# Optimization experiments

Hardware: AMD Instinct MI355X
Metric: run time of the kernel (lower is better)

Reference implementation:

```python
import jax, jax.numpy as jnp
import numpy as np

# RVQECell configuration (matches init_kwargs)
I_SZ, W_SZ, STAGES, ORDER, DEGREE = 6, 12, 3, 2, 2
BIAS = float(np.pi / 2)
ANC = ORDER - 1                      # ancillas_for_order(order) = order - 1
N = I_SZ + W_SZ + ANC                # 19 qubits
B = 32
INOUT = list(range(I_SZ))            # lanes 0..5
WORK = list(range(I_SZ, I_SZ + W_SZ))  # lanes 6..17
C_CTRL = I_SZ + W_SZ - 1             # controls per neuron = 17


def setup_inputs() -> dict:
    key = jax.random.key(0)
    ks = jax.random.split(key, 9)
    s = 0.1  # small init keeps neuron angles in a well-conditioned range
    psi = jax.random.normal(ks[0], (B, 2 ** N), jnp.float32)
    psi = psi / jnp.linalg.norm(psi, axis=1, keepdims=True)  # normalized kets
    return {
        "batch": psi,
        "w_in1": jax.random.normal(ks[1], (W_SZ, C_CTRL), jnp.float32) * s,
        "w_in2": jax.random.normal(ks[2], (W_SZ, C_CTRL, C_CTRL), jnp.float32) * s,
        "w_u": jax.random.normal(ks[3], (STAGES, W_SZ), jnp.float32) * s,
        "w_k1": jax.random.normal(ks[4], (STAGES, W_SZ, C_CTRL), jnp.float32) * s,
        "w_k2": jax.random.normal(ks[5], (STAGES, W_SZ, C_CTRL, C_CTRL), jnp.float32) * s,
        "w_out1": jax.random.normal(ks[6], (I_SZ, C_CTRL), jnp.float32) * s,
        "w_out2": jax.random.normal(ks[7], (I_SZ, C_CTRL, C_CTRL), jnp.float32) * s,
        "inputs": jax.random.randint(ks[8], (B, I_SZ), 0, 2, dtype=jnp.int32),
    }


def _rot_y(state, lane, alpha):
    # real rotation [[cos a, -sin a], [sin a, cos a]] on qubit `lane`.
    ax = lane + 1  # +1 for batch axis; state shape [B] + [2]*N
    c, s = jnp.cos(alpha), jnp.sin(alpha)
    p0 = jax.lax.index_in_dim(state, 0, ax, keepdims=True)
    p1 = jax.lax.index_in_dim(state, 1, ax, keepdims=True)
    return jnp.concatenate([c * p0 - s * p1, s * p0 + c * p1], axis=ax)


def _neuron(state, outlane, th1, th2):
    # Fast (deterministic RUS) quantum neuron of given ORDER/DEGREE:
    # per control-basis-branch rotation of `outlane` by alpha(x),
    # phi(x) = bias + sum_i th1_i x_i + sum_{i<j} th2_ij x_i x_j (degree 2),
    # alpha = q^(order-1)(phi), q(t) = arctan(tan(t)^2), stable via arctan2.
    controls = [l for l in range(I_SZ + W_SZ) if l != outlane]
    Cn = len(controls)
    x = jnp.arange(2 ** Cn)
    shifts = jnp.arange(Cn - 1, -1, -1)
    bits = ((x[:, None] >> shifts[None, :]) & 1).astype(state.dtype)  # [2^Cn, Cn]
    phi = BIAS + bits @ th1
    if DEGREE >= 2:
        phi = phi + jnp.einsum('xi,ij,xj->x', bits, jnp.triu(th2, 1), bits)
    alpha = phi
    for _ in range(ORDER - 1):
        alpha = jnp.arctan2(jnp.sin(alpha) ** 2, jnp.cos(alpha) ** 2)
    shape = [1] + [2 if l in controls else 1 for l in range(N)]
    return _rot_y(state, outlane, alpha.reshape(shape))


def _bitflip(state_flat, inputs):
    # Vectorized batched BitFlipLayer: X on inout lane i where inputs[b,i]==1,
    # i.e. permute amplitudes by XOR of the flip mask (lane 0 most significant).
    shifts = (N - 1) - jnp.arange(I_SZ)
    f = jnp.sum(inputs.astype(jnp.int32) << shifts[None, :], axis=1)  # [B]
    idx = jnp.arange(2 ** N, dtype=jnp.int32)[None, :] ^ f[:, None]
    return jnp.take_along_axis(state_flat, idx, axis=1)


def reference(batch, w_in1, w_in2, w_u, w_k1, w_k2, w_out1, w_out2, inputs):
    psi = _bitflip(batch, inputs).reshape((B,) + (2,) * N)
    # input layer: one neuron per workspace lane
    for j, out in enumerate(WORK):
        psi = _neuron(psi, out, w_in1[j], w_in2[j])
    # kernel layer: stages x (UnitaryLayer(workspace) + neurons)
    for st in range(STAGES):
        for j, lane in enumerate(WORK):
            psi = _rot_y(psi, lane, w_u[st, j])
        for j, out in enumerate(WORK):
            psi = _neuron(psi, out, w_k1[st, j], w_k2[st, j])
    psi = _bitflip(psi.reshape(B, -1), inputs).reshape((B,) + (2,) * N)
    # output layer: one neuron per inout lane
    for j, out in enumerate(INOUT):
        psi = _neuron(psi, out, w_out1[j], w_out2[j])
    # measurement probabilities over inout lanes: marginal of |amp|^2
    probs = jnp.sum(psi ** 2, axis=tuple(range(1 + I_SZ, 1 + N))).reshape(B, -1)
    return probs, psi.reshape(B, -1)
```

## Files before the change

### kernel.cpp

```cpp
#include <hip/hip_runtime.h>
#include <math.h>


#define BIAS_F 1.57079632679489662f

typedef float v4f __attribute__((ext_vector_type(4)));

__device__ __forceinline__ float4 ntload4(const float* p) {
    v4f v = __builtin_nontemporal_load((const v4f*)p);
    return make_float4(v.x, v.y, v.z, v.w);
}
__device__ __forceinline__ void ntstore4(float* p, float4 f) {
    v4f v = {f.x, f.y, f.z, f.w};
    __builtin_nontemporal_store(v, (v4f*)p);
}

__device__ __forceinline__ int SW(int i) { return i ^ ((i >> 3) & 0x1C); }
__device__ __forceinline__ float4 ldsld4(const float* st, int i) {
    return *(const float4*)&st[SW(i)];
}
__device__ __forceinline__ void ldsst4(float* st, int i, float4 v) {
    *(float4*)&st[SW(i)] = v;
}

__device__ __forceinline__ float2 dec(float v) {
    float t = sqrtf(fmaf(-v, v, 1.0f));
    float c = v >= 0.f ? v : t;
    float s = v >= 0.f ? t : -v;
    return make_float2(c, s);
}
#define LD2(p) (*(const float2*)(p))
#define LD4(p) (*(const float4*)(p))

__device__ __forceinline__ void rot4(float4& A, float4& B, float4 e) {
    float ax = A.x, ay = A.y, az = A.z, aw = A.w;
    A.x = e.x * ax - e.y * B.x;  B.x = e.y * ax + e.x * B.x;
    A.y = e.x * ay - e.y * B.y;  B.y = e.y * ay + e.x * B.y;
    A.z = e.z * az - e.w * B.z;  B.z = e.w * az + e.z * B.z;
    A.w = e.z * aw - e.w * B.w;  B.w = e.w * aw + e.z * B.w;
}
__device__ __forceinline__ void rotq(float4& P, float c, float s) {
    float px = P.x, py = P.y;
    P.x = c * px - s * P.z;  P.z = s * px + c * P.z;
    P.y = c * py - s * P.w;  P.w = s * py + c * P.w;
}

#define TABU_FLOATS (48u * 131072u * 2u)

__global__ __launch_bounds__(256) void tables_kernel(
    const float* __restrict__ w_in1, const float* __restrict__ w_in2,
    const float* __restrict__ w_k1,  const float* __restrict__ w_k2,
    const float* __restrict__ w_out1, const float* __restrict__ w_out2,
    float* __restrict__ tab)
{
    const int n = blockIdx.y;
    const int hi = blockIdx.x;
    const int tid = threadIdx.x;
    const float* th1;
    const float* th2;
    if (n < 12)      { th1 = w_in1 + n * 17;         th2 = w_in2 + n * 289; }
    else if (n < 48) { th1 = w_k1 + (n - 12) * 17;   th2 = w_k2 + (n - 12) * 289; }
    else             { th1 = w_out1 + (n - 48) * 17; th2 = w_out2 + (n - 48) * 289; }

    float bu[9], bt[8];
#pragma unroll
    for (int i = 0; i < 9; ++i) bu[i] = (float)((hi >> (8 - i)) & 1);
#pragma unroll
    for (int j = 0; j < 8; ++j) bt[j] = (float)((tid >> (7 - j)) & 1);

    float phi = BIAS_F;
#pragma unroll
    for (int i = 0; i < 9; ++i) {
        float acc = th1[i];
#pragma unroll
        for (int j = i + 1; j < 9; ++j) acc += bu[j] * th2[i * 17 + j];
#pragma unroll
        for (int j = 0; j < 8; ++j)     acc += bt[j] * th2[i * 17 + 9 + j];
        phi += bu[i] * acc;
    }
#pragma unroll
    for (int a = 0; a < 8; ++a) {
        float acc = th1[9 + a];
#pragma unroll
        for (int b2 = a + 1; b2 < 8; ++b2) acc += bt[b2] * th2[(9 + a) * 17 + 9 + b2];
        phi += bt[a] * acc;
    }
    float sp, cp;
    sincosf(phi, &sp, &cp);
    float c2 = cp * cp, s2 = sp * sp;
    float d = c2 * c2 + s2 * s2;
    float r = rsqrtf(d);
    r = r * (1.5f - 0.5f * d * r * r);
    float ca = c2 * r, sa = s2 * r;
    const int idx = (hi << 8) | tid;
    if (n < 48) {
        float2* p = (float2*)tab + ((size_t)n * 131072 + idx);
        *p = make_float2(ca, sa);
    } else {
        tab[TABU_FLOATS + (size_t)(n - 48) * 131072 + idx] = (ca <= sa) ? ca : -sa;
    }
}

template <int PA, bool NEUR>
__device__ __forceinline__ void pass_hi2(float* l0, float* l1, int t8,
    const float* tA, const float* tB, const float* tC,
    float cA, float sA, float cB, float sB, float cC, float sC)
{
    const int lowb = PA - 4;
    const int low = t8 & ((1 << lowb) - 1);
    const int high = t8 >> lowb;
    const int i0 = (high << (PA + 1)) | (low << 2);
    const int x0 = (high << (PA - 1)) | (low << 1);
    const int oa = 1 << PA, ob = oa >> 1, oc = oa >> 2;
    const int dhi = oa >> 2, dlo = oa >> 3;
    float4 ea00, ea01, ea10, ea11, eb00, eb01, eb10, eb11, ec00, ec01, ec10, ec11;
    if (NEUR) {
        ea00 = LD4(&tA[2 * x0]);            ea01 = LD4(&tA[2 * (x0 + dlo)]);
        ea10 = LD4(&tA[2 * (x0 + dhi)]);    ea11 = LD4(&tA[2 * (x0 + dhi + dlo)]);
        eb00 = LD4(&tB[2 * x0]);            eb01 = LD4(&tB[2 * (x0 + dlo)]);
        eb10 = LD4(&tB[2 * (x0 + dhi)]);    eb11 = LD4(&tB[2 * (x0 + dhi + dlo)]);
        ec00 = LD4(&tC[2 * x0]);            ec01 = LD4(&tC[2 * (x0 + dlo)]);
        ec10 = LD4(&tC[2 * (x0 + dhi)]);    ec11 = LD4(&tC[2 * (x0 + dhi + dlo)]);
    } else {
        ea00 = ea01 = ea10 = ea11 = make_float4(cA, sA, cA, sA);
        eb00 = eb01 = eb10 = eb11 = make_float4(cB, sB, cB, sB);
        ec00 = ec01 = ec10 = ec11 = make_float4(cC, sC, cC, sC);
    }
#pragma unroll
    for (int s = 0; s < 2; ++s) {
        float* sl = (s == 0) ? l0 : l1;
        float4 Q000 = ldsld4(sl, i0),            Q001 = ldsld4(sl, i0 + oc);
        float4 Q010 = ldsld4(sl, i0 + ob),       Q011 = ldsld4(sl, i0 + ob + oc);
        float4 Q100 = ldsld4(sl, i0 + oa),       Q101 = ldsld4(sl, i0 + oa + oc);
        float4 Q110 = ldsld4(sl, i0 + oa + ob),  Q111 = ldsld4(sl, i0 + oa + ob + oc);
        rot4(Q000, Q100, ea00); rot4(Q001, Q101, ea01);
        rot4(Q010, Q110, ea10); rot4(Q011, Q111, ea11);
        rot4(Q000, Q010, eb00); rot4(Q001, Q011, eb01);
        rot4(Q100, Q110, eb10); rot4(Q101, Q111, eb11);
        rot4(Q000, Q001, ec00); rot4(Q010, Q011, ec01);
        rot4(Q100, Q101, ec10); rot4(Q110, Q111, ec11);
        ldsst4(sl, i0, Q000);            ldsst4(sl, i0 + oc, Q001);
        ldsst4(sl, i0 + ob, Q010);       ldsst4(sl, i0 + ob + oc, Q011);
        ldsst4(sl, i0 + oa, Q100);       ldsst4(sl, i0 + oa + oc, Q101);
        ldsst4(sl, i0 + oa + ob, Q110);  ldsst4(sl, i0 + oa + ob + oc, Q111);
    }
}

template <bool NEUR>
__device__ __forceinline__ void pass_lo2(float* l0, float* l1, int t8,
    const float* tA, const float* tB, const float* tC,
    float cA, float sA, float cB, float sB, float cC, float sC)
{
    const int i0 = t8 << 5, x0 = t8 << 3;
    float4 ea0, ea1, ea2, ea3, eb0, eb1, eb2, eb3, ec0, ec1, ec2, ec3;
    if (NEUR) {
        ea0 = LD4(&tA[2 * x0]);      ea1 = LD4(&tA[2 * x0 + 4]);
        ea2 = LD4(&tA[2 * x0 + 8]);  ea3 = LD4(&tA[2 * x0 + 12]);
        eb0 = LD4(&tB[2 * x0]);      eb1 = LD4(&tB[2 * x0 + 4]);
        eb2 = LD4(&tB[2 * x0 + 8]);  eb3 = LD4(&tB[2 * x0 + 12]);
        ec0 = LD4(&tC[2 * x0]);      ec1 = LD4(&tC[2 * x0 + 4]);
        ec2 = LD4(&tC[2 * x0 + 8]);  ec3 = LD4(&tC[2 * x0 + 12]);
    } else {
        ea0 = ea1 = ea2 = ea3 = make_float4(cA, sA, cA, sA);
        eb0 = eb1 = eb2 = eb3 = make_float4(cB, sB, cB, sB);
        ec0 = ec1 = ec2 = ec3 = make_float4(cC, sC, cC, sC);
    }
#pragma unroll
    for (int s = 0; s < 2; ++s) {
        float* sl = (s == 0) ? l0 : l1;
        float4 Q0 = ldsld4(sl, i0),      Q1 = ldsld4(sl, i0 + 4);
        float4 Q2 = ldsld4(sl, i0 + 8),  Q3 = ldsld4(sl, i0 + 12);
        float4 Q4 = ldsld4(sl, i0 + 16), Q5 = ldsld4(sl, i0 + 20);
        float4 Q6 = ldsld4(sl, i0 + 24), Q7 = ldsld4(sl, i0 + 28);
        rot4(Q0, Q2, ea0); rot4(Q1, Q3, ea1); rot4(Q4, Q6, ea2); rot4(Q5, Q7, ea3);
        rot4(Q0, Q1, eb0); rot4(Q2, Q3, eb1); rot4(Q4, Q5, eb2); rot4(Q6, Q7, eb3);
        rotq(Q0, ec0.x, ec0.y); rotq(Q1, ec0.z, ec0.w);
        rotq(Q2, ec1.x, ec1.y); rotq(Q3, ec1.z, ec1.w);
        rotq(Q4, ec2.x, ec2.y); rotq(Q5, ec2.z, ec2.w);
        rotq(Q6, ec3.x, ec3.y); rotq(Q7, ec3.z, ec3.w);
        ldsst4(sl, i0, Q0);      ldsst4(sl, i0 + 4, Q1);
        ldsst4(sl, i0 + 8, Q2);  ldsst4(sl, i0 + 12, Q3);
        ldsst4(sl, i0 + 16, Q4); ldsst4(sl, i0 + 20, Q5);
        ldsst4(sl, i0 + 24, Q6); ldsst4(sl, i0 + 28, Q7);
    }
}

__global__ __launch_bounds__(256, 2) void main_kernel(
    const float* __restrict__ batch, const float* __restrict__ w_u,
    const int* __restrict__ inputs, const float* __restrict__ tab,
    float* __restrict__ psi, float* __restrict__ probs)
{
    __shared__ __align__(16) float lds[2][8192];
    const int t8 = threadIdx.x;
    const int blk = blockIdx.x;
    const int xcd = blk & 7;
    const int vt = (xcd << 3) | ((blk >> 3) & 7);
    const int pair = blk >> 6;

    if (blk == 0) {
        float4 z = make_float4(0.f, 0.f, 0.f, 0.f);
        *(float4*)&probs[t8 * 8] = z;
        *(float4*)&probs[t8 * 8 + 4] = z;
    }

    int bb[2], uu[2];
#pragma unroll
    for (int s = 0; s < 2; ++s) {
        int b = pair * 2 + s;
        int fb = 0;
#pragma unroll
        for (int i = 0; i < 6; ++i) fb |= (inputs[b * 6 + i] & 1) << (5 - i);
        bb[s] = b; uu[s] = vt ^ fb;
        const float* src = batch + ((size_t)b << 19) + ((size_t)uu[s] << 13);
#pragma unroll
        for (int k = 0; k < 8; ++k) {
            int i4 = (k * 256 + t8) * 4;
            float4 v = ntload4(&src[i4]);
            *(float4*)&lds[s][SW(i4)] = v;
        }
    }
    float* l0 = lds[0];
    float* l1 = lds[1];

    const float* tb = tab + ((size_t)vt << 12);
#define TN(j) (tb + (size_t)(j) * 262144)
#define BAR __syncthreads()
    BAR;
    pass_hi2<12, true>(l0, l1, t8, TN(0), TN(1), TN(2), 0,0,0,0,0,0);  BAR;
    pass_hi2<9,  true>(l0, l1, t8, TN(3), TN(4), TN(5), 0,0,0,0,0,0);  BAR;
    pass_hi2<6,  true>(l0, l1, t8, TN(6), TN(7), TN(8), 0,0,0,0,0,0);  BAR;
    pass_lo2<true>(l0, l1, t8, TN(9), TN(10), TN(11), 0,0,0,0,0,0);    BAR;

#pragma unroll 1
    for (int st2 = 0; st2 < 3; ++st2) {
        const float* wu = w_u + st2 * 12;
        float c0, s0, c1, s1, c2, s2;
        sincosf(wu[0], &s0, &c0); sincosf(wu[1], &s1, &c1); sincosf(wu[2], &s2, &c2);
        pass_hi2<12, false>(l0, l1, t8, 0,0,0, c0,s0, c1,s1, c2,s2);   BAR;
        sincosf(wu[3], &s0, &c0); sincosf(wu[4], &s1, &c1); sincosf(wu[5], &s2, &c2);
        pass_hi2<9, false>(l0, l1, t8, 0,0,0, c0,s0, c1,s1, c2,s2);    BAR;
        sincosf(wu[6], &s0, &c0); sincosf(wu[7], &s1, &c1); sincosf(wu[8], &s2, &c2);
        pass_hi2<6, false>(l0, l1, t8, 0,0,0, c0,s0, c1,s1, c2,s2);    BAR;
        sincosf(wu[9], &s0, &c0); sincosf(wu[10], &s1, &c1); sincosf(wu[11], &s2, &c2);
        pass_lo2<false>(l0, l1, t8, 0,0,0, c0,s0, c1,s1, c2,s2);       BAR;

        const int nb = 12 + st2 * 12;
        pass_hi2<12, true>(l0, l1, t8, TN(nb+0), TN(nb+1), TN(nb+2), 0,0,0,0,0,0); BAR;
        pass_hi2<9,  true>(l0, l1, t8, TN(nb+3), TN(nb+4), TN(nb+5), 0,0,0,0,0,0); BAR;
        pass_hi2<6,  true>(l0, l1, t8, TN(nb+6), TN(nb+7), TN(nb+8), 0,0,0,0,0,0); BAR;
        pass_lo2<true>(l0, l1, t8, TN(nb+9), TN(nb+10), TN(nb+11), 0,0,0,0,0,0);   BAR;
    }
#undef TN
#undef BAR

#pragma unroll
    for (int s = 0; s < 2; ++s) {
        float* dst = psi + ((size_t)bb[s] << 19) + ((size_t)uu[s] << 13);
#pragma unroll
        for (int k = 0; k < 8; ++k) {
            int i4 = (k * 256 + t8) * 4;
            float4 v = *(const float4*)&lds[s][SW(i4)];
            ntstore4(&dst[i4], v);
        }
    }
}

__global__ __launch_bounds__(256, 2) void out_kernel(
    const float* __restrict__ tab, float* __restrict__ psi,
    float* __restrict__ probs)
{
    __shared__ __align__(16) float ts[16384];
    const int tid = threadIdx.x;
    const int lane = tid & 63;
    const int wv = tid >> 6;
    const int b = blockIdx.x >> 5;
    const int c0 = (blockIdx.x & 31) << 8;
    float* gbase = psi + ((size_t)b << 19) + c0;
    const float* tabp = tab + TABU_FLOATS;

#pragma unroll
    for (int i = 0; i < 16; ++i) {
        int k = wv * 16 + i;
        float4 v = ntload4(&gbase[((size_t)k << 13) + lane * 4]);
        int f4 = lane ^ (k & 15);
        *(float4*)&ts[k * 256 + f4 * 4] = v;
    }
    __syncthreads();

    float a[64];
#pragma unroll
    for (int k = 0; k < 64; ++k) a[k] = ts[k * 256 + (tid ^ ((k & 15) << 2))];
    const int w12 = (c0 | tid) >> 1;

#define OSTAGE(J) { \
    const float* tj = tabp + (size_t)(J) * 131072 + w12; \
    float ev[32]; \
    _Pragma("unroll") \
    for (int m = 0; m < 32; ++m) ev[m] = tj[(size_t)m << 12]; \
    _Pragma("unroll") \
    for (int m = 0; m < 32; ++m) { \
        const int q = 5 - (J); \
        const int k0 = ((m >> q) << (q + 1)) | (m & ((1 << q) - 1)); \
        const int k1 = k0 | (1 << q); \
        float2 e = dec(ev[m]); \
        float A0 = a[k0], A1 = a[k1]; \
        a[k0] = e.x * A0 - e.y * A1; \
        a[k1] = e.y * A0 + e.x * A1; } }
    OSTAGE(0) OSTAGE(1) OSTAGE(2) OSTAGE(3) OSTAGE(4) OSTAGE(5)
#undef OSTAGE

#pragma unroll
    for (int k = 0; k < 64; ++k) ts[k * 256 + (tid ^ ((k & 15) << 2))] = a[k];
    __syncthreads();

#pragma unroll
    for (int i = 0; i < 16; ++i) {
        int k = wv * 16 + i;
        int f4 = lane ^ (k & 15);
        float4 v = *(const float4*)&ts[k * 256 + f4 * 4];
        ntstore4(&gbase[((size_t)k << 13) + lane * 4], v);
    }

    const int k6 = tid & 63, seg = tid >> 6;
    float p = 0.f;
#pragma unroll
    for (int j = 0; j < 64; ++j) {
        int c = seg * 64 + ((j + k6) & 63);
        float v = ts[k6 * 256 + (c ^ ((k6 & 15) << 2))];
        p += v * v;
    }
    atomicAdd(&probs[b * 64 + k6], p);
}

extern "C" void kernel_launch(void* const* d_in, const int* in_sizes, int n_in,
                              void* d_out, int out_size, void* d_ws, size_t ws_size,
                              hipStream_t stream)
{
    const float* batch  = (const float*)d_in[0];
    const float* w_in1  = (const float*)d_in[1];
    const float* w_in2  = (const float*)d_in[2];
    const float* w_u    = (const float*)d_in[3];
    const float* w_k1   = (const float*)d_in[4];
    const float* w_k2   = (const float*)d_in[5];
    const float* w_out1 = (const float*)d_in[6];
    const float* w_out2 = (const float*)d_in[7];
    const int*   inputs = (const int*)d_in[8];
    float* probs = (float*)d_out;
    float* psi   = (float*)d_out + 2048;
    float* tab   = (float*)d_ws;

    tables_kernel<<<dim3(512, 54), 256, 0, stream>>>(w_in1, w_in2, w_k1, w_k2,
                                                     w_out1, w_out2, tab);
    main_kernel<<<1024, 256, 0, stream>>>(batch, w_u, inputs, tab, psi, probs);
    out_kernel<<<1024, 256, 0, stream>>>(tab, psi, probs);
}
```

Before: 351.0 us.

## Hoist high-bit phase terms and store output tables as float2 pairs

The tables kernel now accumulates the high-bit contribution to phi using branches on the block's bits and folds the cross terms into per-low-bit coefficients. This cuts the per-thread multiply-adds. The output-layer table is stored as a full (cos, sin) float2 like the other neurons, so out_kernel no longer runs a sqrt-based decode per element. The cost is twice the table memory and twice the load traffic for the six output stages, with the loads split into two halves to limit register pressure.

```diff
diff --git a/kernel.cpp b/kernel.cpp
--- a/kernel.cpp
+++ b/kernel.cpp
@@ -23,12 +23,6 @@
     *(float4*)&st[SW(i)] = v;
 }
 
-__device__ __forceinline__ float2 dec(float v) {
-    float t = sqrtf(fmaf(-v, v, 1.0f));
-    float c = v >= 0.f ? v : t;
-    float s = v >= 0.f ? t : -v;
-    return make_float2(c, s);
-}
 #define LD2(p) (*(const float2*)(p))
 #define LD4(p) (*(const float4*)(p))
 
@@ -45,7 +39,6 @@
     P.y = c * py - s * P.w;  P.w = s * py + c * P.w;
 }
 
-#define TABU_FLOATS (48u * 131072u * 2u)
 
 __global__ __launch_bounds__(256) void tables_kernel(
     const float* __restrict__ w_in1, const float* __restrict__ w_in2,
@@ -62,43 +55,43 @@
     else if (n < 48) { th1 = w_k1 + (n - 12) * 17;   th2 = w_k2 + (n - 12) * 289; }
     else             { th1 = w_out1 + (n - 48) * 17; th2 = w_out2 + (n - 48) * 289; }
 
-    float bu[9], bt[8];
-#pragma unroll
-    for (int i = 0; i < 9; ++i) bu[i] = (float)((hi >> (8 - i)) & 1);
+    float phi_hi = BIAS_F;
+    float C[8];
+#pragma unroll
+    for (int a = 0; a < 8; ++a) C[a] = th1[9 + a];
+#pragma unroll
+    for (int i = 0; i < 9; ++i) {
+        if ((hi >> (8 - i)) & 1) {
+            float acc = th1[i];
+#pragma unroll
+            for (int j = i + 1; j < 9; ++j)
+                if ((hi >> (8 - j)) & 1) acc += th2[i * 17 + j];
+            phi_hi += acc;
+#pragma unroll
+            for (int a = 0; a < 8; ++a) C[a] += th2[i * 17 + 9 + a];
+        }
+    }
+
+    float bt[8];
 #pragma unroll
     for (int j = 0; j < 8; ++j) bt[j] = (float)((tid >> (7 - j)) & 1);
-
-    float phi = BIAS_F;
-#pragma unroll
-    for (int i = 0; i < 9; ++i) {
-        float acc = th1[i];
-#pragma unroll
-        for (int j = i + 1; j < 9; ++j) acc += bu[j] * th2[i * 17 + j];
-#pragma unroll
-        for (int j = 0; j < 8; ++j)     acc += bt[j] * th2[i * 17 + 9 + j];
-        phi += bu[i] * acc;
-    }
+    float phi = phi_hi;
 #pragma unroll
     for (int a = 0; a < 8; ++a) {
-        float acc = th1[9 + a];
+        float acc = C[a];
 #pragma unroll
         for (int b2 = a + 1; b2 < 8; ++b2) acc += bt[b2] * th2[(9 + a) * 17 + 9 + b2];
         phi += bt[a] * acc;
     }
+
     float sp, cp;
     sincosf(phi, &sp, &cp);
     float c2 = cp * cp, s2 = sp * sp;
     float d = c2 * c2 + s2 * s2;
     float r = rsqrtf(d);
     r = r * (1.5f - 0.5f * d * r * r);
-    float ca = c2 * r, sa = s2 * r;
-    const int idx = (hi << 8) | tid;
-    if (n < 48) {
-        float2* p = (float2*)tab + ((size_t)n * 131072 + idx);
-        *p = make_float2(ca, sa);
-    } else {
-        tab[TABU_FLOATS + (size_t)(n - 48) * 131072 + idx] = (ca <= sa) ? ca : -sa;
-    }
+    float2* dst = (float2*)tab + ((size_t)n * 131072 + (size_t)((hi << 8) | tid));
+    *dst = make_float2(c2 * r, s2 * r);
 }
 
 template <int PA, bool NEUR>
@@ -276,7 +269,6 @@
     const int b = blockIdx.x >> 5;
     const int c0 = (blockIdx.x & 31) << 8;
     float* gbase = psi + ((size_t)b << 19) + c0;
-    const float* tabp = tab + TABU_FLOATS;
 
 #pragma unroll
     for (int i = 0; i < 16; ++i) {
@@ -293,19 +285,22 @@
     const int w12 = (c0 | tid) >> 1;
 
 #define OSTAGE(J) { \
-    const float* tj = tabp + (size_t)(J) * 131072 + w12; \
-    float ev[32]; \
+    const float* tj = tab + 2u * ((size_t)(48 + (J)) * 131072 + (size_t)w12); \
     _Pragma("unroll") \
-    for (int m = 0; m < 32; ++m) ev[m] = tj[(size_t)m << 12]; \
-    _Pragma("unroll") \
-    for (int m = 0; m < 32; ++m) { \
-        const int q = 5 - (J); \
-        const int k0 = ((m >> q) << (q + 1)) | (m & ((1 << q) - 1)); \
-        const int k1 = k0 | (1 << q); \
-        float2 e = dec(ev[m]); \
-        float A0 = a[k0], A1 = a[k1]; \
-        a[k0] = e.x * A0 - e.y * A1; \
-        a[k1] = e.y * A0 + e.x * A1; } }
+    for (int h = 0; h < 2; ++h) { \
+        float2 ev[16]; \
+        _Pragma("unroll") \
+        for (int m = 0; m < 16; ++m) ev[m] = LD2(&tj[(size_t)(h * 16 + m) << 13]); \
+        _Pragma("unroll") \
+        for (int m = 0; m < 16; ++m) { \
+            const int mm = h * 16 + m; \
+            const int q = 5 - (J); \
+            const int k0 = ((mm >> q) << (q + 1)) | (mm & ((1 << q) - 1)); \
+            const int k1 = k0 | (1 << q); \
+            float2 e = ev[m]; \
+            float A0 = a[k0], A1 = a[k1]; \
+            a[k0] = e.x * A0 - e.y * A1; \
+            a[k1] = e.y * A0 + e.x * A1; } } }
     OSTAGE(0) OSTAGE(1) OSTAGE(2) OSTAGE(3) OSTAGE(4) OSTAGE(5)
 #undef OSTAGE
 
```

Result: faster. 328.3 us (-6.5%).
